# Kernel tuning notes

Hardware: AMD Instinct MI355X
Metric: run time of the kernel (lower is better)

## Reference

```python
import jax, jax.numpy as jnp
import numpy as np

B, N, E, H = 2, 20000, 400000, 128
COORDS_WEIGHT = 1.0


def setup_inputs() -> dict:
    key = jax.random.key(0)
    ks = jax.random.split(key, 12)

    def lin(k, i, o, scale=1.0):
        return (jax.random.normal(k, (i, o), jnp.float32) / np.sqrt(i)) * scale

    return {
        "h": jax.random.normal(ks[0], (B, N, H), jnp.float32),
        "coord": jax.random.normal(ks[1], (B, N, 3), jnp.float32),
        "others": jax.random.normal(ks[2], (B, N, H), jnp.float32),
        "edge_index": jax.random.randint(ks[3], (2, E), 0, N),
        "edge_w1": lin(ks[4], 2 * H + 1, H),
        "edge_b1": jnp.zeros((H,), jnp.float32),
        "edge_w2": lin(ks[5], H, H),
        "edge_b2": jnp.zeros((H,), jnp.float32),
        "node_w1": lin(ks[6], 3 * H, H),
        "node_b1": jnp.zeros((H,), jnp.float32),
        "node_w2": lin(ks[7], H, H),
        "node_b2": jnp.zeros((H,), jnp.float32),
        "coord_w1": lin(ks[8], H, H),
        "coord_b1": jnp.zeros((H,), jnp.float32),
        "coord_w2": lin(ks[9], H, 1, scale=0.001),  # xavier gain=0.001, no bias
    }


def reference(h, coord, others, edge_index, edge_w1, edge_b1, edge_w2, edge_b2,
              node_w1, node_b1, node_w2, node_b2, coord_w1, coord_b1, coord_w2):
    row, col = edge_index[0], edge_index[1]
    n_nodes = h.shape[1]

    # coord2radial_X: per-edge coordinate difference and squared distance
    coord_diff = coord[:, row] - coord[:, col]               # [B, E, 3]
    radial = jnp.sum(coord_diff ** 2, axis=-1, keepdims=True)  # [B, E, 1]

    # edge_model_X: gather endpoints, concat with radial, 2-layer ReLU MLP
    src, tgt = h[:, row], h[:, col]                          # [B, E, H]
    e = jnp.concatenate([src, tgt, radial], axis=-1)         # [B, E, 2H+1]
    e = jax.nn.relu(e @ edge_w1 + edge_b1)
    edge_feat = jax.nn.relu(e @ edge_w2 + edge_b2)           # [B, E, H]

    # coord_model_X: trans = coord_diff * coord_mlp(edge_feat); segment-mean over row
    gate = jax.nn.relu(edge_feat @ coord_w1 + coord_b1) @ coord_w2  # [B, E, 1]
    trans = coord_diff * gate                                # [B, E, 3]
    agg_t = jnp.zeros_like(coord).at[:, row].add(trans)      # [B, N, 3]
    cnt = jnp.zeros((n_nodes, 1), coord.dtype).at[row].add(1.0)
    cnt = jnp.maximum(cnt, 1.0)
    f = (agg_t / cnt) * COORDS_WEIGHT
    coord_out = coord + f                                    # [B, N, 3]

    # node_model_X: unsorted_segment_sum over row, concat [others, h, agg], MLP + residual
    agg = jnp.zeros_like(h).at[:, row].add(edge_feat)        # [B, N, H]
    a = jnp.concatenate([others, h, agg], axis=-1)           # [B, N, 3H]
    o = jax.nn.relu(a @ node_w1 + node_b1) @ node_w2 + node_b2
    h_out = h + o                                            # recurrent residual

    # pack node features and coordinates into one output array [B, N, H+3]
    return jnp.concatenate([h_out, coord_out], axis=-1)
```

## Files before the change

kernel.cpp:

```cpp
#include <hip/hip_runtime.h>
#include <cstddef>

#define BN 2
#define NN 20000
#define NE 400000
#define HH 128

typedef __attribute__((ext_vector_type(8))) short bf16x8;
typedef __attribute__((ext_vector_type(4))) float f32x4;
typedef unsigned short ushort_t;

__device__ __forceinline__ unsigned short f2b(float f) {
    unsigned u = __float_as_uint(f);
    unsigned r = (u + 0x7FFFu + ((u >> 16) & 1u)) >> 16;
    return (unsigned short)r;
}
__device__ __forceinline__ float b2f(ushort_t v) {
    return __uint_as_float(((unsigned)v) << 16);
}

__device__ __forceinline__ void gll16(const void* g, void* l) {
    __builtin_amdgcn_global_load_lds(
        (const __attribute__((address_space(1))) unsigned int*)g,
        (__attribute__((address_space(3))) unsigned int*)l,
        16, 0, 0);
}

__global__ void cvt_h_kernel(const float4* __restrict__ src, uint2* __restrict__ dst, int n4) {
    int i = blockIdx.x * 256 + threadIdx.x;
    if (i >= n4) return;
    float4 v = src[i];
    uint2 o;
    o.x = (unsigned)f2b(v.x) | ((unsigned)f2b(v.y) << 16);
    o.y = (unsigned)f2b(v.z) | ((unsigned)f2b(v.w) << 16);
    dst[i] = o;
}

__global__ void pack_w_kernel(const float* __restrict__ W, ushort_t* __restrict__ dst, int K) {
    int slot = blockIdx.x * 256 + threadIdx.x;
    int total = (K >> 6) * 1024;
    if (slot >= total) return;
    int l = slot & 63, nt = (slot >> 6) & 7, kt2 = (slot >> 9) & 1, c = slot >> 10;
    int col = nt * 16 + (l & 15);
    int k0 = c * 64 + kt2 * 32 + ((l >> 4) * 8);
    unsigned out[4];
    #pragma unroll
    for (int p = 0; p < 4; ++p) {
        unsigned lo = f2b(W[(size_t)(k0 + 2 * p) * HH + col]);
        unsigned hi = f2b(W[(size_t)(k0 + 2 * p + 1) * HH + col]);
        out[p] = lo | (hi << 16);
    }
    uint4* d = (uint4*)&dst[(size_t)slot * 8];
    *d = make_uint4(out[0], out[1], out[2], out[3]);
}

__global__ void hist_kernel(const int* __restrict__ eidx, int* __restrict__ histI) {
    int e = blockIdx.x * 256 + threadIdx.x;
    if (e >= NE) return;
    atomicAdd(&histI[eidx[e]], 1);
}

__global__ void scan_kernel(const int* __restrict__ histI, int* __restrict__ cursor,
                            float* __restrict__ cnt) {
    __shared__ int part[256];
    const int t = threadIdx.x;
    const int chunk = (NN + 255) / 256;
    const int lo = t * chunk, hi = min(lo + chunk, NN);
    int s = 0;
    for (int i = lo; i < hi; ++i) s += histI[i];
    part[t] = s;
    __syncthreads();
    for (int d = 1; d < 256; d <<= 1) {
        int v = (t >= d) ? part[t - d] : 0;
        __syncthreads();
        part[t] += v;
        __syncthreads();
    }
    int run = part[t] - s;
    for (int i = lo; i < hi; ++i) {
        cursor[i] = run;
        int hv = histI[i];
        cnt[i] = (float)hv;
        run += hv;
    }
}

__global__ void scatter_kernel(const int* __restrict__ eidx, int* __restrict__ cursor,
                               int* __restrict__ perm) {
    int e = blockIdx.x * 256 + threadIdx.x;
    if (e >= NE) return;
    int p = atomicAdd(&cursor[eidx[e]], 1);
    perm[p] = e;
}

#define MFMA_FA(BB)                                                               \
    _Pragma("unroll")                                                             \
    for (int ktg = 0; ktg < 4; ++ktg) {                                           \
        _Pragma("unroll")                                                         \
        for (int mt = 0; mt < 8; ++mt) {                                          \
            bf16x8 a = *(const bf16x8*)&FA[((ktg * 8 + mt) * 64 + l) * 8];        \
            acc[mt][0] = __builtin_amdgcn_mfma_f32_16x16x32_bf16(                 \
                a, bw[(BB) + ktg * 2 + 0], acc[mt][0], 0, 0, 0);                  \
            acc[mt][1] = __builtin_amdgcn_mfma_f32_16x16x32_bf16(                 \
                a, bw[(BB) + ktg * 2 + 1], acc[mt][1], 0, 0, 0);                  \
        }                                                                         \
    }

#define MFMA_YN(BB)                                                               \
    _Pragma("unroll")                                                             \
    for (int ktg = 0; ktg < 4; ++ktg) {                                           \
        _Pragma("unroll")                                                         \
        for (int mt = 0; mt < 8; ++mt) {                                          \
            const int row_ = mt * 16 + lo16;                                      \
            bf16x8 a = *(const bf16x8*)&YN[row_ * 136 + ktg * 32 + hi4 * 8];      \
            acc[mt][0] = __builtin_amdgcn_mfma_f32_16x16x32_bf16(                 \
                a, bw[(BB) + ktg * 2 + 0], acc[mt][0], 0, 0, 0);                  \
            acc[mt][1] = __builtin_amdgcn_mfma_f32_16x16x32_bf16(                 \
                a, bw[(BB) + ktg * 2 + 1], acc[mt][1], 0, 0, 0);                  \
        }                                                                         \
    }

__global__ __launch_bounds__(256, 2)
void edge_kernel(const ushort_t* __restrict__ hbf, const float* __restrict__ coord,
                 const int* __restrict__ eidx, const int* __restrict__ perm,
                 const ushort_t* __restrict__ w1p, const ushort_t* __restrict__ w2p,
                 const ushort_t* __restrict__ cw1p,
                 const float* __restrict__ w1, const float* __restrict__ b1,
                 const float* __restrict__ b2, const float* __restrict__ cb1,
                 const float* __restrict__ cw2,
                 float* __restrict__ agg, float* __restrict__ aggt)
{
    __shared__ ushort_t FA[4 * 8 * 64 * 8];
    __shared__ ushort_t YN[128 * 136];
    __shared__ int Rw[129], Cw[128];
    __shared__ float CD3[128 * 3];
    __shared__ float Rad[128];
    __shared__ float GT[128];

    const int t = threadIdx.x;
    const int l = t & 63;
    const int w = t >> 6;
    const int b = blockIdx.y;
    const int e0 = blockIdx.x * 128;

    const int lo16 = l & 15;
    const int hi4 = l >> 4;
    const int col0 = w * 32 + lo16;
    const int col1 = col0 + 16;

    bf16x8 bw[16];
    #pragma unroll
    for (int ktg = 0; ktg < 8; ++ktg) {
        bw[ktg * 2 + 0] = *(const bf16x8*)&w1p[((ktg * 8 + w * 2 + 0) * 64 + l) * 8];
        bw[ktg * 2 + 1] = *(const bf16x8*)&w1p[((ktg * 8 + w * 2 + 1) * 64 + l) * 8];
    }

    if (t < 128) {
        const int eid = perm[e0 + t];
        int r = eidx[eid], c = eidx[NE + eid];
        Rw[t] = r; Cw[t] = c; GT[t] = 0.0f;
        if (t == 0) Rw[128] = -1;
        const float* cr = coord + ((size_t)b * NN + r) * 3;
        const float* cc = coord + ((size_t)b * NN + c) * 3;
        float d0 = cr[0] - cc[0], d1 = cr[1] - cc[1], d2 = cr[2] - cc[2];
        CD3[t * 3] = d0; CD3[t * 3 + 1] = d1; CD3[t * 3 + 2] = d2;
        Rad[t] = d0 * d0 + d1 * d1 + d2 * d2;
    }

    f32x4 acc[8][2];
    #pragma unroll
    for (int mt = 0; mt < 8; ++mt) { acc[mt][0] = (f32x4)0.0f; acc[mt][1] = (f32x4)0.0f; }

    __syncthreads();

    #pragma unroll
    for (int i = 0; i < 2; ++i) {
        const int mt = w * 2 + i;
        const ushort_t* hb = hbf + ((size_t)b * NN + Rw[mt * 16 + lo16]) * HH + hi4 * 8;
        #pragma unroll
        for (int ktg = 0; ktg < 4; ++ktg)
            gll16(hb + ktg * 32, (void*)&FA[((ktg * 8 + mt) * 64) * 8]);
    }
    __syncthreads();

    MFMA_FA(0)
    __syncthreads();

    #pragma unroll
    for (int i = 0; i < 2; ++i) {
        const int mt = w * 2 + i;
        const ushort_t* hb = hbf + ((size_t)b * NN + Cw[mt * 16 + lo16]) * HH + hi4 * 8;
        #pragma unroll
        for (int ktg = 0; ktg < 4; ++ktg)
            gll16(hb + ktg * 32, (void*)&FA[((ktg * 8 + mt) * 64) * 8]);
    }
    __syncthreads();

    MFMA_FA(8)

    #pragma unroll
    for (int ktg = 0; ktg < 4; ++ktg) {
        bw[ktg * 2 + 0] = *(const bf16x8*)&w2p[((ktg * 8 + w * 2 + 0) * 64 + l) * 8];
        bw[ktg * 2 + 1] = *(const bf16x8*)&w2p[((ktg * 8 + w * 2 + 1) * 64 + l) * 8];
        bw[8 + ktg * 2 + 0] = *(const bf16x8*)&cw1p[((ktg * 8 + w * 2 + 0) * 64 + l) * 8];
        bw[8 + ktg * 2 + 1] = *(const bf16x8*)&cw1p[((ktg * 8 + w * 2 + 1) * 64 + l) * 8];
    }

    {
        const float w1r0 = w1[256 * HH + col0];
        const float w1r1 = w1[256 * HH + col1];
        const float b10 = b1[col0], b11 = b1[col1];
        #pragma unroll
        for (int mt = 0; mt < 8; ++mt)
            #pragma unroll
            for (int j = 0; j < 4; ++j) {
                const int row = mt * 16 + hi4 * 4 + j;
                const float r = Rad[row];
                float v0 = fmaxf(acc[mt][0][j] + r * w1r0 + b10, 0.0f);
                float v1 = fmaxf(acc[mt][1][j] + r * w1r1 + b11, 0.0f);
                YN[row * 136 + col0] = f2b(v0);
                YN[row * 136 + col1] = f2b(v1);
                acc[mt][0][j] = 0.0f; acc[mt][1][j] = 0.0f;
            }
    }
    __syncthreads();

    MFMA_YN(0)
    __syncthreads();

    {
        const float b20 = b2[col0], b21 = b2[col1];
        #pragma unroll
        for (int mt = 0; mt < 8; ++mt)
            #pragma unroll
            for (int j = 0; j < 4; ++j) {
                const int row = mt * 16 + hi4 * 4 + j;
                float v0 = fmaxf(acc[mt][0][j] + b20, 0.0f);
                float v1 = fmaxf(acc[mt][1][j] + b21, 0.0f);
                YN[row * 136 + col0] = f2b(v0);
                YN[row * 136 + col1] = f2b(v1);
                acc[mt][0][j] = 0.0f; acc[mt][1][j] = 0.0f;
            }
    }
    __syncthreads();

    MFMA_YN(8)

    {
        const int colc = t & 127;
        const int half = t >> 7;
        const int r0 = half * 64;
        float s = 0.0f;
        for (int r = r0; r < r0 + 64; ++r) {
            s += b2f(YN[r * 136 + colc]);
            if (r == r0 + 63 || Rw[r] != Rw[r + 1]) {
                atomicAdd(&agg[((size_t)b * NN + Rw[r]) * HH + colc], s);
                s = 0.0f;
            }
        }
    }

    {
        const float cbA = cb1[col0], cbB = cb1[col1];
        const float cwA = cw2[col0], cwB = cw2[col1];
        #pragma unroll
        for (int mt = 0; mt < 8; ++mt)
            #pragma unroll
            for (int j = 0; j < 4; ++j) {
                float g = fmaxf(acc[mt][0][j] + cbA, 0.0f) * cwA
                        + fmaxf(acc[mt][1][j] + cbB, 0.0f) * cwB;
                g += __shfl_xor(g, 1);
                g += __shfl_xor(g, 2);
                g += __shfl_xor(g, 4);
                g += __shfl_xor(g, 8);
                if (lo16 == 0)
                    atomicAdd(&GT[mt * 16 + hi4 * 4 + j], g);
            }
    }
    __syncthreads();

    if (t < 128) {
        const bool head = (t == 0) || (Rw[t] != Rw[t - 1]);
        if (head) {
            float s0 = 0.0f, s1 = 0.0f, s2 = 0.0f;
            int r = t;
            const int myrow = Rw[t];
            while (r < 128 && Rw[r] == myrow) {
                const float g = GT[r];
                s0 += CD3[r * 3 + 0] * g;
                s1 += CD3[r * 3 + 1] * g;
                s2 += CD3[r * 3 + 2] * g;
                ++r;
            }
            const size_t base = ((size_t)b * NN + myrow) * 3;
            atomicAdd(&aggt[base + 0], s0);
            atomicAdd(&aggt[base + 1], s1);
            atomicAdd(&aggt[base + 2], s2);
        }
    }
}

__global__ __launch_bounds__(256, 2)
void node_kernel(const ushort_t* __restrict__ hbf, const float* __restrict__ h,
                 const float* __restrict__ coord, const float* __restrict__ others,
                 const float* __restrict__ agg,
                 const ushort_t* __restrict__ nw1p, const ushort_t* __restrict__ nw2p,
                 const float* __restrict__ nb1, const float* __restrict__ nb2,
                 const float* __restrict__ aggt, const float* __restrict__ cnt,
                 float* __restrict__ out)
{
    __shared__ ushort_t FA[4 * 8 * 64 * 8];
    __shared__ ushort_t YN[128 * 136];

    const int t = threadIdx.x;
    const int l = t & 63;
    const int w = t >> 6;
    const int b = blockIdx.y;
    const int n0 = blockIdx.x * 128;

    const int lo16 = l & 15;
    const int hi4 = l >> 4;
    const int col0 = w * 32 + lo16;
    const int col1 = col0 + 16;

    bf16x8 bw[24];
    #pragma unroll
    for (int ktg = 0; ktg < 12; ++ktg) {
        bw[ktg * 2 + 0] = *(const bf16x8*)&nw1p[((ktg * 8 + w * 2 + 0) * 64 + l) * 8];
        bw[ktg * 2 + 1] = *(const bf16x8*)&nw1p[((ktg * 8 + w * 2 + 1) * 64 + l) * 8];
    }

    if (t < 128) {
        const int n = n0 + t;
        if (n < NN) {
            const float rinv = 1.0f / fmaxf(cnt[n], 1.0f);
            const float* cp = coord + ((size_t)b * NN + n) * 3;
            const float* ap = aggt + ((size_t)b * NN + n) * 3;
            float* op = out + ((size_t)b * NN + n) * 131 + HH;
            op[0] = cp[0] + ap[0] * rinv;
            op[1] = cp[1] + ap[1] * rinv;
            op[2] = cp[2] + ap[2] * rinv;
        }
    }

    f32x4 acc[8][2];
    #pragma unroll
    for (int mt = 0; mt < 8; ++mt) { acc[mt][0] = (f32x4)0.0f; acc[mt][1] = (f32x4)0.0f; }

    #define STAGE_CVT(SRC)                                                        \
        _Pragma("unroll")                                                         \
        for (int i = 0; i < 2; ++i) {                                             \
            const int mt = w * 2 + i;                                             \
            const int row = min(n0 + mt * 16 + lo16, NN - 1);                     \
            const float* p = (SRC) + ((size_t)b * NN + row) * HH + hi4 * 8;       \
            _Pragma("unroll")                                                     \
            for (int ktg = 0; ktg < 4; ++ktg) {                                   \
                float4 fa = *(const float4*)(p + ktg * 32);                       \
                float4 fb = *(const float4*)(p + ktg * 32 + 4);                   \
                uint4 u;                                                          \
                u.x = (unsigned)f2b(fa.x) | ((unsigned)f2b(fa.y) << 16);          \
                u.y = (unsigned)f2b(fa.z) | ((unsigned)f2b(fa.w) << 16);          \
                u.z = (unsigned)f2b(fb.x) | ((unsigned)f2b(fb.y) << 16);          \
                u.w = (unsigned)f2b(fb.z) | ((unsigned)f2b(fb.w) << 16);          \
                *(uint4*)&FA[((ktg * 8 + mt) * 64 + l) * 8] = u;                  \
            }                                                                     \
        }

    STAGE_CVT(others)
    __syncthreads();
    MFMA_FA(0)
    __syncthreads();

    #pragma unroll
    for (int i = 0; i < 2; ++i) {
        const int mt = w * 2 + i;
        const int row = min(n0 + mt * 16 + lo16, NN - 1);
        const ushort_t* hb = hbf + ((size_t)b * NN + row) * HH + hi4 * 8;
        #pragma unroll
        for (int ktg = 0; ktg < 4; ++ktg)
            gll16(hb + ktg * 32, (void*)&FA[((ktg * 8 + mt) * 64) * 8]);
    }
    __syncthreads();
    MFMA_FA(8)
    __syncthreads();

    STAGE_CVT(agg)
    __syncthreads();
    MFMA_FA(16)

    #pragma unroll
    for (int ktg = 0; ktg < 4; ++ktg) {
        bw[ktg * 2 + 0] = *(const bf16x8*)&nw2p[((ktg * 8 + w * 2 + 0) * 64 + l) * 8];
        bw[ktg * 2 + 1] = *(const bf16x8*)&nw2p[((ktg * 8 + w * 2 + 1) * 64 + l) * 8];
    }

    {
        const float b10 = nb1[col0], b11 = nb1[col1];
        #pragma unroll
        for (int mt = 0; mt < 8; ++mt)
            #pragma unroll
            for (int j = 0; j < 4; ++j) {
                const int row = mt * 16 + hi4 * 4 + j;
                float v0 = fmaxf(acc[mt][0][j] + b10, 0.0f);
                float v1 = fmaxf(acc[mt][1][j] + b11, 0.0f);
                YN[row * 136 + col0] = f2b(v0);
                YN[row * 136 + col1] = f2b(v1);
                acc[mt][0][j] = 0.0f; acc[mt][1][j] = 0.0f;
            }
    }
    __syncthreads();

    MFMA_YN(0)

    {
        const float b20 = nb2[col0], b21 = nb2[col1];
        #pragma unroll
        for (int mt = 0; mt < 8; ++mt)
            #pragma unroll
            for (int j = 0; j < 4; ++j) {
                const int rowg = n0 + mt * 16 + hi4 * 4 + j;
                if (rowg < NN) {
                    const size_t rb = (size_t)b * NN + rowg;
                    out[rb * 131 + col0] = h[rb * HH + col0] + acc[mt][0][j] + b20;
                    out[rb * 131 + col1] = h[rb * HH + col1] + acc[mt][1][j] + b21;
                }
            }
    }
}

extern "C" void kernel_launch(void* const* d_in, const int* in_sizes, int n_in,
                              void* d_out, int out_size, void* d_ws, size_t ws_size,
                              hipStream_t stream)
{
    const float* h      = (const float*)d_in[0];
    const float* coord  = (const float*)d_in[1];
    const float* others = (const float*)d_in[2];
    const int*   eidx   = (const int*)d_in[3];
    const float* w1  = (const float*)d_in[4];
    const float* b1  = (const float*)d_in[5];
    const float* w2  = (const float*)d_in[6];
    const float* b2  = (const float*)d_in[7];
    const float* nw1 = (const float*)d_in[8];
    const float* nb1 = (const float*)d_in[9];
    const float* nw2 = (const float*)d_in[10];
    const float* nb2 = (const float*)d_in[11];
    const float* cw1 = (const float*)d_in[12];
    const float* cb1 = (const float*)d_in[13];
    const float* cw2 = (const float*)d_in[14];
    float* out = (float*)d_out;

    float* agg   = (float*)d_ws;
    float* aggt  = agg + (size_t)BN * NN * HH;
    int*   histI = (int*)(aggt + (size_t)BN * NN * 3);
    float* cnt   = (float*)(histI + NN);
    int*   cursor= (int*)(cnt + NN);
    int*   perm  = cursor + NN;
    ushort_t* hbf  = (ushort_t*)(perm + NE);
    ushort_t* w1p  = hbf + (size_t)BN * NN * HH;
    ushort_t* w2p  = w1p + 32768;
    ushort_t* cw1p = w2p + 16384;
    ushort_t* nw1p = cw1p + 16384;
    ushort_t* nw2p = nw1p + 49152;

    const size_t zero_bytes =
        ((size_t)BN * NN * HH + (size_t)BN * NN * 3 + NN) * sizeof(float);
    hipMemsetAsync(d_ws, 0, zero_bytes, stream);

    const int n4 = (BN * NN * HH) / 4;
    cvt_h_kernel<<<n4 / 256, 256, 0, stream>>>((const float4*)h, (uint2*)hbf, n4);
    pack_w_kernel<<<16, 256, 0, stream>>>(w1, w1p, 256);
    pack_w_kernel<<<8, 256, 0, stream>>>(w2, w2p, 128);
    pack_w_kernel<<<8, 256, 0, stream>>>(cw1, cw1p, 128);
    pack_w_kernel<<<24, 256, 0, stream>>>(nw1, nw1p, 384);
    pack_w_kernel<<<8, 256, 0, stream>>>(nw2, nw2p, 128);

    hist_kernel<<<(NE + 255) / 256, 256, 0, stream>>>(eidx, histI);
    scan_kernel<<<1, 256, 0, stream>>>(histI, cursor, cnt);
    scatter_kernel<<<(NE + 255) / 256, 256, 0, stream>>>(eidx, cursor, perm);

    dim3 eg(NE / 128, BN);
    edge_kernel<<<eg, 256, 0, stream>>>(hbf, coord, eidx, perm, w1p, w2p, cw1p,
                                        w1, b1, b2, cb1, cw2, agg, aggt);

    dim3 ng((NN + 127) / 128, BN);
    node_kernel<<<ng, 256, 0, stream>>>(hbf, h, coord, others, agg,
                                        nw1p, nw2p, nb1, nb2, aggt, cnt, out);
}
```

Before: 586.1 us.

## Alias FA/YN shared buffers, raise edge occupancy, pre-sort row/col indices

```diff
diff --git a/kernel.cpp b/kernel.cpp
--- a/kernel.cpp
+++ b/kernel.cpp
@@ -86,11 +86,13 @@
 }
 
 __global__ void scatter_kernel(const int* __restrict__ eidx, int* __restrict__ cursor,
-                               int* __restrict__ perm) {
+                               int* __restrict__ rowS, int* __restrict__ colS) {
     int e = blockIdx.x * 256 + threadIdx.x;
     if (e >= NE) return;
-    int p = atomicAdd(&cursor[eidx[e]], 1);
-    perm[p] = e;
+    const int r = eidx[e];
+    int p = atomicAdd(&cursor[r], 1);
+    rowS[p] = r;
+    colS[p] = eidx[NE + e];
 }
 
 #define MFMA_FA(BB)                                                               \
@@ -120,9 +122,9 @@
         }                                                                         \
     }
 
-__global__ __launch_bounds__(256, 2)
+__global__ __launch_bounds__(256, 4)
 void edge_kernel(const ushort_t* __restrict__ hbf, const float* __restrict__ coord,
-                 const int* __restrict__ eidx, const int* __restrict__ perm,
+                 const int* __restrict__ rowS, const int* __restrict__ colS,
                  const ushort_t* __restrict__ w1p, const ushort_t* __restrict__ w2p,
                  const ushort_t* __restrict__ cw1p,
                  const float* __restrict__ w1, const float* __restrict__ b1,
@@ -130,12 +132,14 @@
                  const float* __restrict__ cw2,
                  float* __restrict__ agg, float* __restrict__ aggt)
 {
-    __shared__ ushort_t FA[4 * 8 * 64 * 8];
-    __shared__ ushort_t YN[128 * 136];
+    __shared__ ushort_t SH[128 * 136];
     __shared__ int Rw[129], Cw[128];
     __shared__ float CD3[128 * 3];
     __shared__ float Rad[128];
     __shared__ float GT[128];
+
+    ushort_t* const FA = SH;
+    ushort_t* const YN = SH;
 
     const int t = threadIdx.x;
     const int l = t & 63;
@@ -156,8 +160,7 @@
     }
 
     if (t < 128) {
-        const int eid = perm[e0 + t];
-        int r = eidx[eid], c = eidx[NE + eid];
+        int r = rowS[e0 + t], c = colS[e0 + t];
         Rw[t] = r; Cw[t] = c; GT[t] = 0.0f;
         if (t == 0) Rw[128] = -1;
         const float* cr = coord + ((size_t)b * NN + r) * 3;
@@ -205,6 +208,8 @@
         bw[8 + ktg * 2 + 0] = *(const bf16x8*)&cw1p[((ktg * 8 + w * 2 + 0) * 64 + l) * 8];
         bw[8 + ktg * 2 + 1] = *(const bf16x8*)&cw1p[((ktg * 8 + w * 2 + 1) * 64 + l) * 8];
     }
+
+    __syncthreads();
 
     {
         const float w1r0 = w1[256 * HH + col0];
@@ -309,8 +314,9 @@
                  const float* __restrict__ aggt, const float* __restrict__ cnt,
                  float* __restrict__ out)
 {
-    __shared__ ushort_t FA[4 * 8 * 64 * 8];
-    __shared__ ushort_t YN[128 * 136];
+    __shared__ ushort_t SH[128 * 136];
+    ushort_t* const FA = SH;
+    ushort_t* const YN = SH;
 
     const int t = threadIdx.x;
     const int l = t & 63;
@@ -393,6 +399,8 @@
         bw[ktg * 2 + 0] = *(const bf16x8*)&nw2p[((ktg * 8 + w * 2 + 0) * 64 + l) * 8];
         bw[ktg * 2 + 1] = *(const bf16x8*)&nw2p[((ktg * 8 + w * 2 + 1) * 64 + l) * 8];
     }
+
+    __syncthreads();
 
     {
         const float b10 = nb1[col0], b11 = nb1[col1];
@@ -454,8 +462,9 @@
     int*   histI = (int*)(aggt + (size_t)BN * NN * 3);
     float* cnt   = (float*)(histI + NN);
     int*   cursor= (int*)(cnt + NN);
-    int*   perm  = cursor + NN;
-    ushort_t* hbf  = (ushort_t*)(perm + NE);
+    int*   rowS  = cursor + NN;
+    int*   colS  = rowS + NE;
+    ushort_t* hbf  = (ushort_t*)(colS + NE);
     ushort_t* w1p  = hbf + (size_t)BN * NN * HH;
     ushort_t* w2p  = w1p + 32768;
     ushort_t* cw1p = w2p + 16384;
@@ -476,10 +485,10 @@
 
     hist_kernel<<<(NE + 255) / 256, 256, 0, stream>>>(eidx, histI);
     scan_kernel<<<1, 256, 0, stream>>>(histI, cursor, cnt);
-    scatter_kernel<<<(NE + 255) / 256, 256, 0, stream>>>(eidx, cursor, perm);
+    scatter_kernel<<<(NE + 255) / 256, 256, 0, stream>>>(eidx, cursor, rowS, colS);
 
     dim3 eg(NE / 128, BN);
-    edge_kernel<<<eg, 256, 0, stream>>>(hbf, coord, eidx, perm, w1p, w2p, cw1p,
+    edge_kernel<<<eg, 256, 0, stream>>>(hbf, coord, rowS, colS, w1p, w2p, cw1p,
                                         w1, b1, b2, cb1, cw2, agg, aggt);
 
     dim3 ng((NN + 127) / 128, BN);
```

Result: faster. 489.5 us (-16.5%).
